# Performance work log

Measured on AMD Instinct MI355X. Metric: run time of the kernel, lower is better.

## Reference

```python
import jax, jax.numpy as jnp
import numpy as np

NUM_BITS = 4
N_VAL = 2 ** NUM_BITS - 1            # 15
INTERVAL = 2.0 / N_VAL               # init_range / n_val (non-trainable)
ZERO = 0.0                           # self.zero (non-trainable, default init)
EPS = 1e-3


def setup_inputs() -> dict:
    key = jax.random.key(0)
    k1, k2 = jax.random.split(key)
    x = jax.random.normal(k1, (32, 256, 56, 56), dtype=jnp.float32)
    # learned bin widths, initialized near `interval` with some spread
    a = (INTERVAL * (0.8 + 0.4 * jax.random.uniform(k2, (N_VAL,)))).astype(jnp.float32)
    start = jnp.full((1,), -1.0, dtype=jnp.float32)  # quantization range start
    scale1 = jnp.ones((1,), dtype=jnp.float32)
    scale2 = jnp.ones((1,), dtype=jnp.float32)
    return {"x": x, "start": start, "a": a, "scale1": scale1, "scale2": scale2}


def reference(x, start, a, scale1, scale2):
    xs = x * scale1                              # broadcast scalar
    s = start[0]
    a_pos = jnp.where(a > EPS, a, EPS)           # [n_val]
    cums = jnp.cumsum(a_pos)                     # [n_val]
    # thre_backward[i] = start + sum_{j<i} a_pos[j]
    tb = s + jnp.concatenate([jnp.zeros((1,), a_pos.dtype), cums[:-1]])
    # thre_forward[i] = thre_backward[i] + a_pos[i]/2
    tf = tb + a_pos * 0.5
    dt = xs.dtype

    # forward (hard) branch: count of strict exceedances of the sorted tf
    cnt_f = jnp.searchsorted(tf, xs, side="left")        # in [0, n_val]
    x_forward = ZERO + cnt_f.astype(dt) * jnp.asarray(INTERVAL, dt)

    # backward (soft) branch: piecewise-linear interpolation within the active bin
    cnt_b = jnp.searchsorted(tb, xs, side="left")        # in [0, n_val]
    idx = jnp.clip(cnt_b - 1, 0, N_VAL - 1)
    lin = (INTERVAL / a_pos[idx]) * (xs - tb[idx]) + ZERO + idx.astype(dt) * INTERVAL
    x_backward = jnp.where(cnt_b == 0, jnp.asarray(ZERO, dt), lin)
    top = s + cums[-1]                                    # last thre_backward + a_pos[-1]
    x_backward = jnp.where(xs > top, jnp.asarray(2.0, dt), x_backward)

    # straight-through combine: value from x_forward, gradient from x_backward
    out = jax.lax.stop_gradient(x_forward) + x_backward - jax.lax.stop_gradient(x_backward)
    return out * scale2
```

## Files before the change

### kernel.cpp

```cpp
#include <hip/hip_runtime.h>

#define NVAL 15

__global__ __launch_bounds__(256) void ltq_fwd_kernel(
    const float* __restrict__ x,
    const float* __restrict__ start,
    const float* __restrict__ a,
    const float* __restrict__ scale1,
    const float* __restrict__ scale2,
    float* __restrict__ out,
    int n)
{
    const float s   = start[0];
    const float sc1 = scale1[0];
    const float k   = (float)(2.0 / 15.0) * scale2[0];

    float tf[NVAL];
    float cum = 0.0f;
#pragma unroll
    for (int i = 0; i < NVAL; ++i) {
        float ai = a[i];
        float ap = (ai > 1e-3f) ? ai : 1e-3f;
        float tb = s + cum;
        tf[i] = tb + 0.5f * ap;
        cum += ap;
    }

    const int n4 = n >> 2;
    const float4* __restrict__ x4 = (const float4*)x;
    float4* __restrict__ o4 = (float4*)out;
    const int stride = gridDim.x * blockDim.x;

    for (int idx = blockIdx.x * blockDim.x + threadIdx.x; idx < n4; idx += stride) {
        float4 v = x4[idx];
        float xs0 = v.x * sc1;
        float xs1 = v.y * sc1;
        float xs2 = v.z * sc1;
        float xs3 = v.w * sc1;
        int c0 = 0, c1 = 0, c2 = 0, c3 = 0;
#pragma unroll
        for (int i = 0; i < NVAL; ++i) {
            float t = tf[i];
            c0 += (xs0 > t);
            c1 += (xs1 > t);
            c2 += (xs2 > t);
            c3 += (xs3 > t);
        }
        float4 r;
        r.x = k * (float)c0;
        r.y = k * (float)c1;
        r.z = k * (float)c2;
        r.w = k * (float)c3;
        o4[idx] = r;
    }

    const int tail_start = n4 << 2;
    for (int idx = tail_start + blockIdx.x * blockDim.x + threadIdx.x; idx < n; idx += stride) {
        float xs = x[idx] * sc1;
        int c = 0;
#pragma unroll
        for (int i = 0; i < NVAL; ++i) c += (xs > tf[i]);
        out[idx] = k * (float)c;
    }
}

extern "C" void kernel_launch(void* const* d_in, const int* in_sizes, int n_in,
                              void* d_out, int out_size, void* d_ws, size_t ws_size,
                              hipStream_t stream) {
    const float* x      = (const float*)d_in[0];
    const float* start  = (const float*)d_in[1];
    const float* a      = (const float*)d_in[2];
    const float* scale1 = (const float*)d_in[3];
    const float* scale2 = (const float*)d_in[4];
    float* out = (float*)d_out;
    const int n = in_sizes[0];

    ltq_fwd_kernel<<<2048, 256, 0, stream>>>(x, start, a, scale1, scale2, out, n);
}
```

Baseline: 188.5 us.

## Replace grid-stride loop with exact grid, batched 4x loads, nontemporal stores

The persistent grid-stride loop over 2048 blocks is replaced by a grid sized to cover the data once. Each thread issues four independent 16-byte loads up front, strided by T, before computing, which raises memory-level parallelism. Outputs are written with nontemporal stores to reduce cache pollution on this streaming workload. The cost is many more blocks to launch and somewhat more register pressure per thread.

After: 191.7 us. About the same (+1.7%).

```diff
diff --git a/kernel.cpp b/kernel.cpp
--- a/kernel.cpp
+++ b/kernel.cpp
@@ -1,6 +1,9 @@
 #include <hip/hip_runtime.h>
 
 #define NVAL 15
+#define VPT 4
+
+typedef float fvec4 __attribute__((ext_vector_type(4)));
 
 __global__ __launch_bounds__(256) void ltq_fwd_kernel(
     const float* __restrict__ x,
@@ -9,7 +12,7 @@
     const float* __restrict__ scale1,
     const float* __restrict__ scale2,
     float* __restrict__ out,
-    int n)
+    int n, int n4, int T )
 {
     const float s   = start[0];
     const float sc1 = scale1[0];
@@ -26,17 +29,27 @@
         cum += ap;
     }
 
-    const int n4 = n >> 2;
-    const float4* __restrict__ x4 = (const float4*)x;
-    float4* __restrict__ o4 = (float4*)out;
-    const int stride = gridDim.x * blockDim.x;
+    const fvec4* __restrict__ x4 = (const fvec4*)x;
+    fvec4* __restrict__ o4 = (fvec4*)out;
 
-    for (int idx = blockIdx.x * blockDim.x + threadIdx.x; idx < n4; idx += stride) {
-        float4 v = x4[idx];
-        float xs0 = v.x * sc1;
-        float xs1 = v.y * sc1;
-        float xs2 = v.z * sc1;
-        float xs3 = v.w * sc1;
+    const int tid = blockIdx.x * blockDim.x + threadIdx.x;
+
+    fvec4 v[VPT];
+    bool ok[VPT];
+#pragma unroll
+    for (int j = 0; j < VPT; ++j) {
+        int i = tid + j * T;
+        ok[j] = (i < n4);
+        if (ok[j]) v[j] = x4[i];
+    }
+
+#pragma unroll
+    for (int j = 0; j < VPT; ++j) {
+        if (!ok[j]) continue;
+        float xs0 = v[j].x * sc1;
+        float xs1 = v[j].y * sc1;
+        float xs2 = v[j].z * sc1;
+        float xs3 = v[j].w * sc1;
         int c0 = 0, c1 = 0, c2 = 0, c3 = 0;
 #pragma unroll
         for (int i = 0; i < NVAL; ++i) {
@@ -46,16 +59,16 @@
             c2 += (xs2 > t);
             c3 += (xs3 > t);
         }
-        float4 r;
+        fvec4 r;
         r.x = k * (float)c0;
         r.y = k * (float)c1;
         r.z = k * (float)c2;
         r.w = k * (float)c3;
-        o4[idx] = r;
+        __builtin_nontemporal_store(r, &o4[tid + j * T]);
     }
 
     const int tail_start = n4 << 2;
-    for (int idx = tail_start + blockIdx.x * blockDim.x + threadIdx.x; idx < n; idx += stride) {
+    for (int idx = tail_start + tid; idx < n; idx += T * VPT) {
         float xs = x[idx] * sc1;
         int c = 0;
 #pragma unroll
@@ -75,5 +88,10 @@
     float* out = (float*)d_out;
     const int n = in_sizes[0];
 
-    ltq_fwd_kernel<<<2048, 256, 0, stream>>>(x, start, a, scale1, scale2, out, n);
+    const int n4 = n >> 2;
+    const int T  = (n4 + VPT - 1) / VPT;
+    const int threads = 256;
+    const int blocks  = (T + threads - 1) / threads;
+    ltq_fwd_kernel<<<blocks, threads, 0, stream>>>(x, start, a, scale1, scale2,
+                                                   out, n, n4, T);
 }
```
